# Kernel tuning notes

Measured on AMD Instinct MI355X. Metric: run time of the kernel, lower is better.

The kernel has to match this reference:

```python
import jax, jax.numpy as jnp
import numpy as np

Q_MAX = 127.0  # 2**(8-1) - 1
EPS = 1e-08


def quantize_activation(x):
    # per-tensor symmetric int8 quant with STE
    scale = jnp.maximum(jnp.max(jnp.abs(x)) / Q_MAX, EPS)
    x_scaled = x / scale
    rounded = jnp.clip(jnp.round(x_scaled), -Q_MAX, Q_MAX)
    # STE: forward = rounded, backward = identity w.r.t. x_scaled
    q = x_scaled + jax.lax.stop_gradient(rounded - x_scaled)
    return q, jax.lax.stop_gradient(scale)


def ternarize_weight(W):
    scale = jnp.mean(jnp.abs(W)) + EPS
    W_norm = W / scale
    rounded = jnp.clip(jnp.round(W_norm), -1.0, 1.0)
    # STE: forward = rounded, backward = identity w.r.t. W
    tW = W + jax.lax.stop_gradient(rounded - W)
    return tW, jax.lax.stop_gradient(scale)


def setup_inputs() -> dict:
    key = jax.random.key(0)
    kx, kw = jax.random.split(key)
    in_features, out_features = 4096, 11008
    x = jax.random.normal(kx, (4, 2048, in_features), dtype=jnp.float32)
    # kaiming_uniform_(a=sqrt(5)) -> U(-bound, bound), bound = sqrt(6/((1+a^2)*fan_in)) = 1/sqrt(fan_in)
    bound = 1.0 / np.sqrt(in_features)
    W = jax.random.uniform(kw, (out_features, in_features), dtype=jnp.float32,
                           minval=-bound, maxval=bound)
    return {"x": x, "W": W}


def reference(x, W):
    qx, act_scale = quantize_activation(x)
    tW, w_scale = ternarize_weight(W)
    # F.linear: x @ W.T ; [b, s, in] x [out, in] -> [b, s, out]
    out = jnp.einsum('bsi,oi->bso', qx, tW)
    return out * (w_scale * act_scale)
```

## Files before the change

kernel.cpp:

```cpp
#include <hip/hip_runtime.h>
#include <cstdint>

typedef int i32x4 __attribute__((ext_vector_type(4)));
typedef int i32x16 __attribute__((ext_vector_type(16)));

#define M_DIM 8192
#define N_DIM 11008
#define K_DIM 4096

#define WS_AMAX_OFF   0
#define WS_WSUM_OFF   4096
#define WS_SCALES_OFF 12288
#define WS_QX_OFF     16384
#define WS_TW_OFF     (16384 + 33554432)

__device__ __forceinline__ void gload_lds16(const void* g, void* l) {
  __builtin_amdgcn_global_load_lds(
      (const __attribute__((address_space(1))) unsigned int*)g,
      (__attribute__((address_space(3))) unsigned int*)l, 16, 0, 0);
}


__global__ void reduce_amax(const float* __restrict__ x, float* __restrict__ partial, int n4) {
  const float4* xv = (const float4*)x;
  float m = 0.f;
  for (long i = (long)blockIdx.x * blockDim.x + threadIdx.x; i < n4;
       i += (long)gridDim.x * blockDim.x) {
    float4 v = xv[i];
    m = fmaxf(m, fmaxf(fmaxf(fabsf(v.x), fabsf(v.y)), fmaxf(fabsf(v.z), fabsf(v.w))));
  }
  __shared__ float sm[256];
  sm[threadIdx.x] = m;
  __syncthreads();
  for (int s = 128; s > 0; s >>= 1) {
    if (threadIdx.x < s) sm[threadIdx.x] = fmaxf(sm[threadIdx.x], sm[threadIdx.x + s]);
    __syncthreads();
  }
  if (threadIdx.x == 0) partial[blockIdx.x] = sm[0];
}

__global__ void reduce_wsum(const float* __restrict__ w, double* __restrict__ partial, int n4) {
  const float4* wv = (const float4*)w;
  double acc = 0.0;
  for (long i = (long)blockIdx.x * blockDim.x + threadIdx.x; i < n4;
       i += (long)gridDim.x * blockDim.x) {
    float4 v = wv[i];
    acc += (double)fabsf(v.x) + (double)fabsf(v.y) + (double)fabsf(v.z) + (double)fabsf(v.w);
  }
  __shared__ double sd[256];
  sd[threadIdx.x] = acc;
  __syncthreads();
  for (int s = 128; s > 0; s >>= 1) {
    if (threadIdx.x < s) sd[threadIdx.x] += sd[threadIdx.x + s];
    __syncthreads();
  }
  if (threadIdx.x == 0) partial[blockIdx.x] = sd[0];
}

__global__ void finalize_scales(const float* __restrict__ amax_p,
                                const double* __restrict__ wsum_p,
                                float* __restrict__ scales) {
  __shared__ float sm[1024];
  __shared__ double sd[1024];
  const int t = threadIdx.x;
  sm[t] = amax_p[t];
  sd[t] = wsum_p[t];
  __syncthreads();
  for (int s = 512; s > 0; s >>= 1) {
    if (t < s) {
      sm[t] = fmaxf(sm[t], sm[t + s]);
      sd[t] += sd[t + s];
    }
    __syncthreads();
  }
  if (t == 0) {
    float act_scale = fmaxf(sm[0] / 127.0f, 1e-8f);
    float w_scale = (float)(sd[0] / (double)((long long)N_DIM * K_DIM)) + 1e-8f;
    scales[0] = act_scale;
    scales[1] = w_scale;
    scales[2] = act_scale * w_scale;
  }
}


__device__ __forceinline__ int quant_clip(float v, float s, float lim) {
  float r = rintf(v / s);
  r = fminf(fmaxf(r, -lim), lim);
  return (int)r;
}

__global__ void quant_x(const float* __restrict__ x, const float* __restrict__ scales,
                        int8_t* __restrict__ q) {
  const float s = scales[0];
  const long i = (long)blockIdx.x * blockDim.x + threadIdx.x;
  const float4* xv = (const float4*)x + (i << 2);
  i32x4 pk;
#pragma unroll
  for (int j = 0; j < 4; ++j) {
    float4 v = xv[j];
    int b0 = quant_clip(v.x, s, 127.f);
    int b1 = quant_clip(v.y, s, 127.f);
    int b2 = quant_clip(v.z, s, 127.f);
    int b3 = quant_clip(v.w, s, 127.f);
    pk[j] = (b0 & 255) | ((b1 & 255) << 8) | ((b2 & 255) << 16) | (b3 << 24);
  }
  *((i32x4*)q + i) = pk;
}

__global__ void tern_w(const float* __restrict__ w, const float* __restrict__ scales,
                       int8_t* __restrict__ q) {
  const float s = scales[1];
  const long i = (long)blockIdx.x * blockDim.x + threadIdx.x;
  const float4* wv = (const float4*)w + (i << 2);
  i32x4 pk;
#pragma unroll
  for (int j = 0; j < 4; ++j) {
    float4 v = wv[j];
    int b0 = quant_clip(v.x, s, 1.f);
    int b1 = quant_clip(v.y, s, 1.f);
    int b2 = quant_clip(v.z, s, 1.f);
    int b3 = quant_clip(v.w, s, 1.f);
    pk[j] = (b0 & 255) | ((b1 & 255) << 8) | ((b2 & 255) << 16) | (b3 << 24);
  }
  *((i32x4*)q + i) = pk;
}


__global__ __launch_bounds__(256) void gemm_i8(const int8_t* __restrict__ qx,
                                               const int8_t* __restrict__ tw,
                                               const float* __restrict__ scales,
                                               float* __restrict__ out) {
  __shared__ __align__(16) int8_t As[128 * 128];
  __shared__ __align__(16) int8_t Bs[128 * 128];

  const int tid = threadIdx.x;
  const int l = tid & 63;
  const int w = tid >> 6;
  const int wm = (w >> 1) << 6;
  const int wn = (w & 1) << 6;

  const int TN = N_DIM / 128;
  int bid = blockIdx.x;
  int p = bid / (8 * TN);
  int r = bid - p * (8 * TN);
  int mi = (p << 3) + (r & 7);
  int ni = r >> 3;
  const long row0 = (long)mi << 7;
  const long col0 = (long)ni << 7;

  const int srow = l >> 3;
  const int schunk = (l & 7) ^ srow;
  const int8_t* gA = qx + (row0 + (w << 5) + srow) * (long)K_DIM + (schunk << 4);
  const int8_t* gB = tw + (col0 + (w << 5) + srow) * (long)K_DIM + (schunk << 4);
  int8_t* lA = As + ((w << 5) * 128);
  int8_t* lB = Bs + ((w << 5) * 128);

  i32x16 acc[2][2];
#pragma unroll
  for (int i = 0; i < 2; ++i)
#pragma unroll
    for (int j = 0; j < 2; ++j)
#pragma unroll
      for (int e = 0; e < 16; ++e) acc[i][j][e] = 0;

  const int arow = wm + (l & 31);
  const int brow = wn + (l & 31);
  const int asz = arow & 7;
  const int bsz = brow & 7;
  const int khalf = l >> 5;

  for (int kt = 0; kt < K_DIM / 128; ++kt) {
#pragma unroll
    for (int i = 0; i < 4; ++i) {
      gload_lds16(gA + (long)kt * 128 + (long)(i * 8) * K_DIM, lA + i * 8 * 128);
      gload_lds16(gB + (long)kt * 128 + (long)(i * 8) * K_DIM, lB + i * 8 * 128);
    }
    __syncthreads();
#pragma unroll
    for (int kk = 0; kk < 4; ++kk) {
      const int cc = (kk << 1) + khalf;
      i32x4 a0 = *(const i32x4*)(As + arow * 128 + ((cc ^ asz) << 4));
      i32x4 a1 = *(const i32x4*)(As + (arow + 32) * 128 + ((cc ^ asz) << 4));
      i32x4 b0 = *(const i32x4*)(Bs + brow * 128 + ((cc ^ bsz) << 4));
      i32x4 b1 = *(const i32x4*)(Bs + (brow + 32) * 128 + ((cc ^ bsz) << 4));
      acc[0][0] = __builtin_amdgcn_mfma_i32_32x32x32_i8(a0, b0, acc[0][0], 0, 0, 0);
      acc[0][1] = __builtin_amdgcn_mfma_i32_32x32x32_i8(a0, b1, acc[0][1], 0, 0, 0);
      acc[1][0] = __builtin_amdgcn_mfma_i32_32x32x32_i8(a1, b0, acc[1][0], 0, 0, 0);
      acc[1][1] = __builtin_amdgcn_mfma_i32_32x32x32_i8(a1, b1, acc[1][1], 0, 0, 0);
    }
    __syncthreads();
  }

  const float osc = scales[2];
  const int coll = l & 31;
  const int rbase = (l >> 5) << 2;
#pragma unroll
  for (int fi = 0; fi < 2; ++fi)
#pragma unroll
    for (int fj = 0; fj < 2; ++fj)
#pragma unroll
      for (int reg = 0; reg < 16; ++reg) {
        int rr = wm + (fi << 5) + rbase + (reg & 3) + ((reg >> 2) << 3);
        int cc2 = wn + (fj << 5) + coll;
        out[(row0 + rr) * (long)N_DIM + (col0 + cc2)] = (float)acc[fi][fj][reg] * osc;
      }
}


extern "C" void kernel_launch(void* const* d_in, const int* in_sizes, int n_in,
                              void* d_out, int out_size, void* d_ws, size_t ws_size,
                              hipStream_t stream) {
  const float* x = (const float*)d_in[0];
  const float* W = (const float*)d_in[1];
  float* out = (float*)d_out;

  char* ws = (char*)d_ws;
  float*  amax_p = (float*)(ws + WS_AMAX_OFF);
  double* wsum_p = (double*)(ws + WS_WSUM_OFF);
  float*  scales = (float*)(ws + WS_SCALES_OFF);
  int8_t* qx = (int8_t*)(ws + WS_QX_OFF);
  int8_t* tw = (int8_t*)(ws + WS_TW_OFF);

  reduce_amax<<<1024, 256, 0, stream>>>(x, amax_p, (M_DIM * (long)K_DIM) / 4);
  reduce_wsum<<<1024, 256, 0, stream>>>(W, wsum_p, (N_DIM * (long)K_DIM) / 4);
  finalize_scales<<<1, 1024, 0, stream>>>(amax_p, wsum_p, scales);
  quant_x<<<(M_DIM * (long)K_DIM) / 16 / 256, 256, 0, stream>>>(x, scales, qx);
  tern_w<<<(N_DIM * (long)K_DIM) / 16 / 256, 256, 0, stream>>>(W, scales, tw);

  const int grid = (M_DIM / 128) * (N_DIM / 128);
  gemm_i8<<<grid, 256, 0, stream>>>(qx, tw, scales, out);
}
```

Measured before the change: 606.7 us.

## Enlarge int8 GEMM tile to 256x256 with double-buffered LDS pipeline

Rewrites the int8 MFMA GEMM to use 512-thread blocks that each compute a 256x256 output tile, with 8 waves each owning a 128x64 sub-tile. This raises data reuse per LDS load and cuts global traffic per output. The K loop now double-buffers LDS: it prefetches the next K slice with direct global-to-LDS loads while computing on the current one, using explicit vmcnt waits and barriers. It also adds XCD-aware block mapping and s_setprio around the MFMA bursts. The cost is 128KB of LDS per block, which limits occupancy to one block per CU, plus heavier register use for the accumulators.

```diff
diff --git a/kernel.cpp b/kernel.cpp
--- a/kernel.cpp
+++ b/kernel.cpp
@@ -7,6 +7,7 @@
 #define M_DIM 8192
 #define N_DIM 11008
 #define K_DIM 4096
+#define NT    (K_DIM / 128)
 
 #define WS_AMAX_OFF   0
 #define WS_WSUM_OFF   4096
@@ -126,83 +127,118 @@
 }
 
 
-__global__ __launch_bounds__(256) void gemm_i8(const int8_t* __restrict__ qx,
-                                               const int8_t* __restrict__ tw,
-                                               const float* __restrict__ scales,
-                                               float* __restrict__ out) {
-  __shared__ __align__(16) int8_t As[128 * 128];
-  __shared__ __align__(16) int8_t Bs[128 * 128];
+__global__ __launch_bounds__(512, 2) void gemm_i8(const int8_t* __restrict__ qx,
+                                                  const int8_t* __restrict__ tw,
+                                                  const float* __restrict__ scales,
+                                                  float* __restrict__ out) {
+  __shared__ __align__(16) int8_t lds[4][32768];
 
   const int tid = threadIdx.x;
   const int l = tid & 63;
   const int w = tid >> 6;
-  const int wm = (w >> 1) << 6;
-  const int wn = (w & 1) << 6;
-
-  const int TN = N_DIM / 128;
-  int bid = blockIdx.x;
-  int p = bid / (8 * TN);
-  int r = bid - p * (8 * TN);
-  int mi = (p << 3) + (r & 7);
-  int ni = r >> 3;
-  const long row0 = (long)mi << 7;
-  const long col0 = (long)ni << 7;
-
-  const int srow = l >> 3;
-  const int schunk = (l & 7) ^ srow;
-  const int8_t* gA = qx + (row0 + (w << 5) + srow) * (long)K_DIM + (schunk << 4);
-  const int8_t* gB = tw + (col0 + (w << 5) + srow) * (long)K_DIM + (schunk << 4);
-  int8_t* lA = As + ((w << 5) * 128);
-  int8_t* lB = Bs + ((w << 5) * 128);
-
-  i32x16 acc[2][2];
-#pragma unroll
-  for (int i = 0; i < 2; ++i)
-#pragma unroll
-    for (int j = 0; j < 2; ++j)
-#pragma unroll
-      for (int e = 0; e < 16; ++e) acc[i][j][e] = 0;
-
-  const int arow = wm + (l & 31);
-  const int brow = wn + (l & 31);
-  const int asz = arow & 7;
-  const int bsz = brow & 7;
+
+  const int bid = blockIdx.x;
+  const int xcd = bid & 7;
+  const int local = bid >> 3;
+  const int ni = local >> 2;
+  const int mi = (xcd << 2) + (local & 3);
+  const long row0 = (long)mi << 8;
+  const long col0 = (long)ni << 8;
+
+  const int srow = tid >> 3;
+  const int sch = (tid & 7) ^ (srow & 7);
+  const int8_t* pA = qx + (row0 + srow) * (long)K_DIM + (sch << 4);
+  const int8_t* pB = tw + (col0 + srow) * (long)K_DIM + (sch << 4);
+  const int ldst = w << 10;
+
+  auto stage = [&](int8_t* dA, int8_t* dB, int kt) {
+    const long cb = (long)kt << 7;
+#pragma unroll
+    for (int i = 0; i < 4; ++i)
+      gload_lds16(pA + cb + ((long)i * 64) * K_DIM, dA + i * 8192 + ldst);
+#pragma unroll
+    for (int i = 0; i < 4; ++i)
+      gload_lds16(pB + cb + ((long)i * 64) * K_DIM, dB + i * 8192 + ldst);
+  };
+
+  const int lane31 = l & 31;
   const int khalf = l >> 5;
-
-  for (int kt = 0; kt < K_DIM / 128; ++kt) {
-#pragma unroll
-    for (int i = 0; i < 4; ++i) {
-      gload_lds16(gA + (long)kt * 128 + (long)(i * 8) * K_DIM, lA + i * 8 * 128);
-      gload_lds16(gB + (long)kt * 128 + (long)(i * 8) * K_DIM, lB + i * 8 * 128);
+  const int swz = l & 7;
+  int cOff[4];
+#pragma unroll
+  for (int ks = 0; ks < 4; ++ks) cOff[ks] = ((((ks << 1) | khalf) ^ swz) << 4);
+  const int aRow = ((w >> 2) * 128 + lane31) * 128;
+  int bRow[2];
+  bRow[0] = ((w & 3) * 64 + lane31) * 128;
+  bRow[1] = bRow[0] + 32 * 128;
+
+  i32x16 acc[4][2];
+#pragma unroll
+  for (int mf = 0; mf < 4; ++mf)
+#pragma unroll
+    for (int nf = 0; nf < 2; ++nf)
+#pragma unroll
+      for (int e = 0; e < 16; ++e) acc[mf][nf][e] = 0;
+
+  int8_t* cA = lds[0];
+  int8_t* cB = lds[2];
+  int8_t* nA = lds[1];
+  int8_t* nB = lds[3];
+
+  stage(cA, cB, 0);
+
+  for (int kt = 0; kt < NT; ++kt) {
+    if (kt + 1 < NT) {
+      stage(nA, nB, kt + 1);
+      asm volatile("s_waitcnt vmcnt(8)" ::: "memory");
+    } else {
+      asm volatile("s_waitcnt vmcnt(0)" ::: "memory");
     }
-    __syncthreads();
-#pragma unroll
-    for (int kk = 0; kk < 4; ++kk) {
-      const int cc = (kk << 1) + khalf;
-      i32x4 a0 = *(const i32x4*)(As + arow * 128 + ((cc ^ asz) << 4));
-      i32x4 a1 = *(const i32x4*)(As + (arow + 32) * 128 + ((cc ^ asz) << 4));
-      i32x4 b0 = *(const i32x4*)(Bs + brow * 128 + ((cc ^ bsz) << 4));
-      i32x4 b1 = *(const i32x4*)(Bs + (brow + 32) * 128 + ((cc ^ bsz) << 4));
-      acc[0][0] = __builtin_amdgcn_mfma_i32_32x32x32_i8(a0, b0, acc[0][0], 0, 0, 0);
-      acc[0][1] = __builtin_amdgcn_mfma_i32_32x32x32_i8(a0, b1, acc[0][1], 0, 0, 0);
-      acc[1][0] = __builtin_amdgcn_mfma_i32_32x32x32_i8(a1, b0, acc[1][0], 0, 0, 0);
-      acc[1][1] = __builtin_amdgcn_mfma_i32_32x32x32_i8(a1, b1, acc[1][1], 0, 0, 0);
+    __builtin_amdgcn_s_barrier();
+    asm volatile("" ::: "memory");
+
+    i32x4 bf[2][4];
+#pragma unroll
+    for (int nf = 0; nf < 2; ++nf)
+#pragma unroll
+      for (int ks = 0; ks < 4; ++ks)
+        bf[nf][ks] = *(const i32x4*)(cB + bRow[nf] + cOff[ks]);
+
+#pragma unroll
+    for (int mf = 0; mf < 4; ++mf) {
+      i32x4 af[4];
+#pragma unroll
+      for (int ks = 0; ks < 4; ++ks)
+        af[ks] = *(const i32x4*)(cA + aRow + mf * 4096 + cOff[ks]);
+      __builtin_amdgcn_s_setprio(1);
+#pragma unroll
+      for (int ks = 0; ks < 4; ++ks) {
+        acc[mf][0] = __builtin_amdgcn_mfma_i32_32x32x32_i8(af[ks], bf[0][ks], acc[mf][0], 0, 0, 0);
+        acc[mf][1] = __builtin_amdgcn_mfma_i32_32x32x32_i8(af[ks], bf[1][ks], acc[mf][1], 0, 0, 0);
+      }
+      __builtin_amdgcn_s_setprio(0);
     }
-    __syncthreads();
+
+    asm volatile("s_waitcnt lgkmcnt(0)" ::: "memory");
+    __builtin_amdgcn_s_barrier();
+    asm volatile("" ::: "memory");
+
+    int8_t* t;
+    t = cA; cA = nA; nA = t;
+    t = cB; cB = nB; nB = t;
   }
 
   const float osc = scales[2];
-  const int coll = l & 31;
-  const int rbase = (l >> 5) << 2;
-#pragma unroll
-  for (int fi = 0; fi < 2; ++fi)
-#pragma unroll
-    for (int fj = 0; fj < 2; ++fj)
+  const int rbase = khalf << 2;
+#pragma unroll
+  for (int mf = 0; mf < 4; ++mf)
+#pragma unroll
+    for (int nf = 0; nf < 2; ++nf)
 #pragma unroll
       for (int reg = 0; reg < 16; ++reg) {
-        int rr = wm + (fi << 5) + rbase + (reg & 3) + ((reg >> 2) << 3);
-        int cc2 = wn + (fj << 5) + coll;
-        out[(row0 + rr) * (long)N_DIM + (col0 + cc2)] = (float)acc[fi][fj][reg] * osc;
+        int rr = (w >> 2) * 128 + mf * 32 + rbase + (reg & 3) + ((reg >> 2) << 3);
+        int cc = (w & 3) * 64 + nf * 32 + lane31;
+        out[(row0 + rr) * (long)N_DIM + (col0 + cc)] = (float)acc[mf][nf][reg] * osc;
       }
 }
 
@@ -227,6 +263,6 @@
   quant_x<<<(M_DIM * (long)K_DIM) / 16 / 256, 256, 0, stream>>>(x, scales, qx);
   tern_w<<<(N_DIM * (long)K_DIM) / 16 / 256, 256, 0, stream>>>(W, scales, tw);
 
-  const int grid = (M_DIM / 128) * (N_DIM / 128);
-  gemm_i8<<<grid, 256, 0, stream>>>(qx, tw, scales, out);
-}
+  const int grid = (M_DIM / 256) * (N_DIM / 256);
+  gemm_i8<<<grid, 512, 0, stream>>>(qx, tw, scales, out);
+}
```

New measurement: 563.2 us. 1.08x faster.
